# Kernel optimization log

Hardware: AMD Instinct MI355X
Metric: run time of the kernel (lower is better)

Reference implementation:

```python
import jax, jax.numpy as jnp
import numpy as np

# Dimensions (AlphaFold-scale IPA / GeometricFrameAttention)
B, N = 1, 768
C_S, C_Z, C_H, H, PQ, PV = 384, 128, 16, 12, 4, 8
INF = 1e9
EPS = 1e-8
SOFTPLUS_INV_1 = 0.541324854612918  # gfa_point_weights_init_


def quat_to_rot(q):
    """Unit-normalize quaternions [..., 4] -> rotation matrices [..., 3, 3]."""
    q = q / jnp.linalg.norm(q, axis=-1, keepdims=True)
    w, x, y, z = q[..., 0], q[..., 1], q[..., 2], q[..., 3]
    R = jnp.stack([
        1 - 2 * (y * y + z * z), 2 * (x * y - w * z), 2 * (x * z + w * y),
        2 * (x * y + w * z), 1 - 2 * (x * x + z * z), 2 * (y * z - w * x),
        2 * (x * z - w * y), 2 * (y * z + w * x), 1 - 2 * (x * x + y * y),
    ], axis=-1)
    return R.reshape(q.shape[:-1] + (3, 3))


def setup_inputs() -> dict:
    key = jax.random.key(0)
    ks = jax.random.split(key, 12)

    def lin(k, out_d, in_d):
        return jax.random.normal(k, (out_d, in_d), jnp.float32) * (1.0 / np.sqrt(in_d))

    out_in = H * C_H + H * PV * 4 + H * C_Z  # o + o_pt(x,y,z) + o_pt_norm + o_pair
    inp = {
        "s": jax.random.normal(ks[0], (B, N, C_S), jnp.float32),
        "z": jax.random.normal(ks[1], (B, N, N, C_Z), jnp.float32),
        "rot": quat_to_rot(jax.random.normal(ks[2], (B, N, 4), jnp.float32)),
        "trans": jax.random.normal(ks[3], (B, N, 3), jnp.float32),
        "mask": jnp.ones((B, N), jnp.float32),
        "Wq": lin(ks[4], H * C_H, C_S),
        "bq": jnp.zeros((H * C_H,), jnp.float32),
        "Wkv": lin(ks[5], H * 2 * C_H, C_S),
        "bkv": jnp.zeros((H * 2 * C_H,), jnp.float32),
        "Wqp": lin(ks[6], H * PQ * 3, C_S),
        "bqp": jnp.zeros((H * PQ * 3,), jnp.float32),
        "Wkvp": lin(ks[7], H * (PQ + PV) * 3, C_S),
        "bkvp": jnp.zeros((H * (PQ + PV) * 3,), jnp.float32),
        "Wb": lin(ks[8], H, C_Z),
        "bb": jnp.zeros((H,), jnp.float32),
        "head_w": jnp.full((H,), SOFTPLUS_INV_1, jnp.float32),
        "Wout": lin(ks[9], C_S, out_in),
        "bout": jnp.zeros((C_S,), jnp.float32),
    }
    return inp


def _forward(s, z, rot, trans, mask, Wq, bq, Wkv, bkv, Wqp, bqp, Wkvp, bkvp,
             Wb, bb, head_w, Wout, bout):
    Bn, Nn, _ = s.shape
    # scalar q/k/v
    q = (s @ Wq.T + bq).reshape(Bn, Nn, H, C_H)
    kv = (s @ Wkv.T + bkv).reshape(Bn, Nn, H, 2 * C_H)
    k, v = kv[..., :C_H], kv[..., C_H:]
    # point q/k/v: local frame -> global frame (x_glob = R x_loc + t)
    q_pts = (s @ Wqp.T + bqp).reshape(Bn, Nn, H * PQ, 3)
    q_pts = (jnp.einsum('bnxy,bnpy->bnpx', rot, q_pts) + trans[:, :, None]).reshape(Bn, Nn, H, PQ, 3)
    kv_pts = (s @ Wkvp.T + bkvp).reshape(Bn, Nn, H * (PQ + PV), 3)
    kv_pts = (jnp.einsum('bnxy,bnpy->bnpx', rot, kv_pts) + trans[:, :, None]).reshape(Bn, Nn, H, PQ + PV, 3)
    k_pts, v_pts = kv_pts[..., :PQ, :], kv_pts[..., PQ:, :]
    # pair bias [B,N,N,H] -> [B,H,N,N]
    bias = z @ Wb.T + bb
    a = jnp.einsum('bihc,bjhc->bhij', q, k) * np.float32(np.sqrt(1.0 / (3 * C_H)))
    a = a + np.float32(np.sqrt(1.0 / 3.0)) * jnp.transpose(bias, (0, 3, 1, 2))
    # point distance term: sum_p |q_p - k_p|^2 = |q|^2 + |k|^2 - 2 q.k (no [B,N,N,H,P,3] tensor)
    q2 = jnp.sum(q_pts ** 2, axis=(-1, -2))  # [B,N,H]
    k2 = jnp.sum(k_pts ** 2, axis=(-1, -2))
    qk = jnp.einsum('bihpc,bjhpc->bhij', q_pts, k_pts)
    d2 = q2.transpose(0, 2, 1)[..., :, None] + k2.transpose(0, 2, 1)[..., None, :] - 2.0 * qk
    hw = jax.nn.softplus(head_w) * np.float32(np.sqrt(2.0 / (27.0 * PQ)))  # sqrt(1/(3*(PQ*9/2)))
    a = a - 0.5 * hw[None, :, None, None] * d2
    # mask bias
    sq_mask = mask[..., :, None] * mask[..., None, :]
    a = a + (INF * (sq_mask - 1.0))[:, None]
    a = jax.nn.softmax(a, axis=-1)  # [B,H,N,N]
    # outputs
    o = jnp.einsum('bhij,bjhc->bihc', a, v).reshape(Bn, Nn, H * C_H)
    o_pt = jnp.einsum('bhij,bjhpc->bihpc', a, v_pts)  # global frame
    o_pt = jnp.einsum('bnyx,bnhpy->bnhpx', rot, o_pt - trans[:, :, None, None])  # back to local
    o_pt_norm = jnp.sqrt(jnp.sum(o_pt ** 2, axis=-1) + EPS).reshape(Bn, Nn, H * PV)
    o_pt_flat = jnp.moveaxis(o_pt, -1, -3).reshape(Bn, Nn, 3 * H * PV)  # coord-major like unbind+cat
    o_pair = jnp.einsum('bhij,bijc->bihc', a, z).reshape(Bn, Nn, H * C_Z)
    cat = jnp.concatenate([o, o_pt_flat, o_pt_norm, o_pair], axis=-1)
    return cat @ Wout.T + bout


def reference(s, z, rot, trans, mask, Wq, bq, Wkv, bkv, Wqp, bqp, Wkvp, bkvp,
              Wb, bb, head_w, Wout, bout):
    return _forward(s, z, rot, trans, mask, Wq, bq, Wkv, bkv, Wqp, bqp,
                    Wkvp, bkvp, Wb, bb, head_w, Wout, bout)
```

## Files before the change

### kernel.cpp

```cpp
#include <hip/hip_runtime.h>
#include <math.h>

#define NN 768
#define CS 384
#define CZ 128
#define CH 16
#define HH 12
#define PQ 4
#define PV 8
#define OUTIN 2112

#define SC_QK 0.14433756729740643f
#define SC_B  0.57735026918962576f
#define SC_HW 0.13608276348795434f

__global__ __launch_bounds__(256) void kproj(
    const float* __restrict__ s,
    const float* __restrict__ Wq,  const float* __restrict__ bq,
    const float* __restrict__ Wkv, const float* __restrict__ bkv,
    const float* __restrict__ Wqp, const float* __restrict__ bqp,
    const float* __restrict__ Wkvp,const float* __restrict__ bkvp,
    float* __restrict__ q, float* __restrict__ kT, float* __restrict__ vallT,
    float* __restrict__ qpr, float* __restrict__ kvpr)
{
    __shared__ float s_lds[8*384];
    int n0 = blockIdx.x * 8;
    int t = threadIdx.x;
    for (int idx = t; idx < 8*384; idx += 256)
        s_lds[idx] = s[(n0 + idx/384)*384 + (idx%384)];
    __syncthreads();

    int o = blockIdx.y * 128 + (t & 127);
    int ng = t >> 7;
    const float* wrow; float bias;
    if (o < 192)      { wrow = Wq   + o*384;       bias = bq[o]; }
    else if (o < 576) { wrow = Wkv  + (o-192)*384; bias = bkv[o-192]; }
    else if (o < 720) { wrow = Wqp  + (o-576)*384; bias = bqp[o-576]; }
    else              { wrow = Wkvp + (o-720)*384; bias = bkvp[o-720]; }

    float acc[4] = {bias, bias, bias, bias};
    const float4* wr4 = reinterpret_cast<const float4*>(wrow);
    for (int c4 = 0; c4 < 96; ++c4) {
        float4 w = wr4[c4];
        #pragma unroll
        for (int nn = 0; nn < 4; ++nn) {
            const float* sr = &s_lds[(ng*4+nn)*384 + c4*4];
            acc[nn] = fmaf(w.x, sr[0], acc[nn]);
            acc[nn] = fmaf(w.y, sr[1], acc[nn]);
            acc[nn] = fmaf(w.z, sr[2], acc[nn]);
            acc[nn] = fmaf(w.w, sr[3], acc[nn]);
        }
    }
    #pragma unroll
    for (int nn = 0; nn < 4; ++nn) {
        int n = n0 + ng*4 + nn;
        float v = acc[nn];
        if (o < 192)      q[n*192 + o] = v;
        else if (o < 576) {
            int oo = o - 192, h = oo >> 5, cc = oo & 31;
            if (cc < 16) kT[(h*NN + n)*16 + cc] = v;
            else         vallT[(size_t)(h*40 + (cc-16))*NN + n] = v;
        }
        else if (o < 720) qpr[n*144 + (o-576)] = v;
        else              kvpr[n*432 + (o-720)] = v;
    }
}

__global__ __launch_bounds__(192) void krot(
    const float* __restrict__ rot, const float* __restrict__ trans,
    const float* __restrict__ qpr, const float* __restrict__ kvpr,
    float* __restrict__ qp, float* __restrict__ kpT, float* __restrict__ vallT)
{
    int n = blockIdx.x;
    __shared__ float R[9], T[3];
    int t = threadIdx.x;
    if (t < 9) R[t] = rot[n*9 + t];
    if (t < 3) T[t] = trans[n*3 + t];
    __syncthreads();

    const float* src = (t < 48) ? (qpr + n*144 + t*3) : (kvpr + n*432 + (t-48)*3);
    float x = src[0], y = src[1], z = src[2];
    float wx = R[0]*x + R[1]*y + R[2]*z + T[0];
    float wy = R[3]*x + R[4]*y + R[5]*z + T[1];
    float wz = R[6]*x + R[7]*y + R[8]*z + T[2];
    if (t < 48) {
        float* d = qp + n*144 + t*3;
        d[0]=wx; d[1]=wy; d[2]=wz;
    } else {
        int pi = t - 48, h = pi/12, pp = pi%12;
        if (pp < 4) {
            float* d = kpT + (h*NN+n)*12 + pp*3;
            d[0]=wx; d[1]=wy; d[2]=wz;
        } else {
            int ch = h*40 + 16 + (pp-4)*3;
            vallT[(size_t)(ch+0)*NN + n] = wx;
            vallT[(size_t)(ch+1)*NN + n] = wy;
            vallT[(size_t)(ch+2)*NN + n] = wz;
        }
    }
}

__global__ __launch_bounds__(256) void kqk(
    const float* __restrict__ kT, const float* __restrict__ kpT,
    const float* __restrict__ q, const float* __restrict__ qp,
    const float* __restrict__ mask, const float* __restrict__ head_w,
    const float* __restrict__ bb, float* __restrict__ lqd)
{
    const int h = blockIdx.z;
    const int j0 = blockIdx.x * 128;
    const int i0 = blockIdx.y * 32;
    __shared__ float kt_l[16][132], kp_l[12][132];
    __shared__ float q_l[32][16], qp_l[32][12];
    __shared__ float mi_l[32], mj_l[128];
    const int t = threadIdx.x;
    for (int idx = t; idx < 2048; idx += 256) {
        int j = idx >> 4, c = idx & 15;
        kt_l[c][j] = kT[(size_t)(h*NN + j0 + j)*16 + c];
    }
    for (int idx = t; idx < 1536; idx += 256) {
        int j = idx / 12, e = idx - j*12;
        kp_l[e][j] = kpT[(size_t)(h*NN + j0 + j)*12 + e];
    }
    for (int idx = t; idx < 512; idx += 256) {
        int ii = idx >> 4, c = idx & 15;
        q_l[ii][c] = q[(i0+ii)*192 + h*16 + c];
    }
    for (int idx = t; idx < 384; idx += 256) {
        int ii = idx / 12, e = idx - ii*12;
        qp_l[ii][e] = qp[(i0+ii)*144 + h*12 + e];
    }
    if (t < 32)  mi_l[t] = mask[i0 + t];
    if (t < 128) mj_l[t] = mask[j0 + t];
    const float hwh = log1pf(expf(head_w[h])) * SC_HW;
    const float bbh = bb[h];
    __syncthreads();

    const int jl = t & 127, ig = t >> 7;
    const float mj = mj_l[jl];
    #pragma unroll 4
    for (int ii = 0; ii < 16; ++ii) {
        const int il = ig*16 + ii;
        float qk = 0.f;
        #pragma unroll
        for (int c = 0; c < 16; ++c) qk = fmaf(kt_l[c][jl], q_l[il][c], qk);
        float d2 = 0.f;
        #pragma unroll
        for (int e = 0; e < 12; ++e) { float d = qp_l[il][e] - kp_l[e][jl]; d2 = fmaf(d, d, d2); }
        float mt = 1e9f * (mi_l[il]*mj - 1.0f);
        float lg = fmaf(qk, SC_QK, fmaf(-0.5f*hwh, d2, bbh)) + mt;
        lqd[((size_t)h*NN + i0 + il)*NN + j0 + jl] = lg;
    }
}

__global__ __launch_bounds__(256, 4) void kbias(
    const float* __restrict__ z, const float* __restrict__ Wb,
    const float* __restrict__ lqd, float* __restrict__ g_out,
    float* __restrict__ mrow)
{
    __shared__ float4 zt4[64][32];

    const int i = blockIdx.x, t = threadIdx.x;
    const int w = t >> 6, l = t & 63, h0 = w*3;
    const int h0u = __builtin_amdgcn_readfirstlane(h0);
    const float4* __restrict__ wbh = (const float4*)(Wb + h0u*CZ);

    const float4* __restrict__ zg = (const float4*)(z + (size_t)i*NN*CZ);
    float4 stg[8];
    #pragma unroll
    for (int k = 0; k < 8; ++k) stg[k] = zg[k*256 + t];
    #pragma unroll
    for (int k = 0; k < 8; ++k) {
        int slot = k*256 + t, j = slot >> 5, c4 = slot & 31;
        zt4[j][c4 ^ (j & 7)] = stg[k];
    }

    float m0 = -1e30f, m1 = -1e30f, m2 = -1e30f;
    const int swl = l & 7;

    for (int tile = 0; tile < 12; ++tile) {
        __syncthreads();
        if (tile + 1 < 12) {
            #pragma unroll
            for (int k = 0; k < 8; ++k) stg[k] = zg[(tile+1)*2048 + k*256 + t];
        }
        const int j = tile*64 + l;
        float lq0 = lqd[((size_t)(h0+0)*NN + i)*NN + j];
        float lq1 = lqd[((size_t)(h0+1)*NN + i)*NN + j];
        float lq2 = lqd[((size_t)(h0+2)*NN + i)*NN + j];
        float b0 = 0.f, b1 = 0.f, b2 = 0.f;
        #pragma unroll
        for (int c4 = 0; c4 < 32; ++c4) {
            float4 zv = zt4[l][c4 ^ swl];
            float4 w0 = wbh[c4];
            float4 w1 = wbh[32 + c4];
            float4 w2 = wbh[64 + c4];
            b0 = fmaf(zv.x,w0.x,b0); b0 = fmaf(zv.y,w0.y,b0); b0 = fmaf(zv.z,w0.z,b0); b0 = fmaf(zv.w,w0.w,b0);
            b1 = fmaf(zv.x,w1.x,b1); b1 = fmaf(zv.y,w1.y,b1); b1 = fmaf(zv.z,w1.z,b1); b1 = fmaf(zv.w,w1.w,b1);
            b2 = fmaf(zv.x,w2.x,b2); b2 = fmaf(zv.y,w2.y,b2); b2 = fmaf(zv.z,w2.z,b2); b2 = fmaf(zv.w,w2.w,b2);
        }
        float g0 = fmaf(b0, SC_B, lq0);
        float g1 = fmaf(b1, SC_B, lq1);
        float g2 = fmaf(b2, SC_B, lq2);
        g_out[((size_t)(h0+0)*NN + i)*NN + j] = g0;
        g_out[((size_t)(h0+1)*NN + i)*NN + j] = g1;
        g_out[((size_t)(h0+2)*NN + i)*NN + j] = g2;
        m0 = fmaxf(m0, g0); m1 = fmaxf(m1, g1); m2 = fmaxf(m2, g2);
        __syncthreads();
        if (tile + 1 < 12) {
            #pragma unroll
            for (int k = 0; k < 8; ++k) {
                int slot = k*256 + t, jj = slot >> 5, c4 = slot & 31;
                zt4[jj][c4 ^ (jj & 7)] = stg[k];
            }
        }
    }

    #pragma unroll
    for (int off = 32; off >= 1; off >>= 1) {
        m0 = fmaxf(m0, __shfl_xor(m0, off, 64));
        m1 = fmaxf(m1, __shfl_xor(m1, off, 64));
        m2 = fmaxf(m2, __shfl_xor(m2, off, 64));
    }
    if (l == 0) {
        mrow[(h0+0)*NN + i] = m0;
        mrow[(h0+1)*NN + i] = m1;
        mrow[(h0+2)*NN + i] = m2;
    }
}

__global__ __launch_bounds__(256, 4) void kfin(
    const float* __restrict__ z, const float* __restrict__ vallT,
    const float* __restrict__ g, const float* __restrict__ mrow,
    const float* __restrict__ rot, const float* __restrict__ trans,
    float* __restrict__ cat)
{
    __shared__ float an_l[12][776];
    __shared__ float sred[12][4];
    __shared__ float sinv[12];
    __shared__ float optl[12][24];
    __shared__ float R[9], T[3];
    const int i = blockIdx.x, t = threadIdx.x, w = t >> 6, l = t & 63;
    if (t < 9) R[t] = rot[i*9 + t];
    if (t < 3) T[t] = trans[i*3 + t];

    float ps[12];
    #pragma unroll
    for (int h = 0; h < 12; ++h) ps[h] = 0.f;
    #pragma unroll
    for (int h = 0; h < 12; ++h) {
        const float mh = mrow[h*NN + i];
        const float* gr = g + ((size_t)h*NN + i)*NN;
        #pragma unroll
        for (int k = 0; k < 3; ++k) {
            int j = k*256 + t;
            float p = __expf(gr[j] - mh);
            an_l[h][j] = p;
            ps[h] += p;
        }
    }
    #pragma unroll
    for (int h = 0; h < 12; ++h) {
        float s = ps[h];
        #pragma unroll
        for (int off = 32; off >= 1; off >>= 1) s += __shfl_xor(s, off, 64);
        if (l == 0) sred[h][w] = s;
    }
    __syncthreads();
    if (t < 12) sinv[t] = 1.0f / (sred[t][0] + sred[t][1] + sred[t][2] + sred[t][3]);
    __syncthreads();

    {
        const int h0 = w*3, jo = l >> 5, c4 = l & 31;
        const float4* __restrict__ zr = (const float4*)(z + (size_t)i*NN*CZ);
        float a0x=0,a0y=0,a0z=0,a0w=0, a1x=0,a1y=0,a1z=0,a1w=0, a2x=0,a2y=0,a2z=0,a2w=0;
        #pragma unroll 4
        for (int jb = 0; jb < 384; ++jb) {
            const int j = jb*2 + jo;
            float4 zv = zr[(size_t)j*32 + c4];
            float p0 = an_l[h0+0][j], p1 = an_l[h0+1][j], p2 = an_l[h0+2][j];
            a0x = fmaf(p0, zv.x, a0x); a0y = fmaf(p0, zv.y, a0y);
            a0z = fmaf(p0, zv.z, a0z); a0w = fmaf(p0, zv.w, a0w);
            a1x = fmaf(p1, zv.x, a1x); a1y = fmaf(p1, zv.y, a1y);
            a1z = fmaf(p1, zv.z, a1z); a1w = fmaf(p1, zv.w, a1w);
            a2x = fmaf(p2, zv.x, a2x); a2y = fmaf(p2, zv.y, a2y);
            a2z = fmaf(p2, zv.z, a2z); a2w = fmaf(p2, zv.w, a2w);
        }
        a0x += __shfl_xor(a0x, 32, 64); a0y += __shfl_xor(a0y, 32, 64);
        a0z += __shfl_xor(a0z, 32, 64); a0w += __shfl_xor(a0w, 32, 64);
        a1x += __shfl_xor(a1x, 32, 64); a1y += __shfl_xor(a1y, 32, 64);
        a1z += __shfl_xor(a1z, 32, 64); a1w += __shfl_xor(a1w, 32, 64);
        a2x += __shfl_xor(a2x, 32, 64); a2y += __shfl_xor(a2y, 32, 64);
        a2z += __shfl_xor(a2z, 32, 64); a2w += __shfl_xor(a2w, 32, 64);
        if (jo == 0) {
            float* crow = cat + (size_t)i*OUTIN + 576;
            float i0v = sinv[h0+0], i1v = sinv[h0+1], i2v = sinv[h0+2];
            float4 o0; o0.x = a0x*i0v; o0.y = a0y*i0v; o0.z = a0z*i0v; o0.w = a0w*i0v;
            float4 o1; o1.x = a1x*i1v; o1.y = a1y*i1v; o1.z = a1z*i1v; o1.w = a1w*i1v;
            float4 o2; o2.x = a2x*i2v; o2.y = a2y*i2v; o2.z = a2z*i2v; o2.w = a2w*i2v;
            *(float4*)(crow + (h0+0)*128 + c4*4) = o0;
            *(float4*)(crow + (h0+1)*128 + c4*4) = o1;
            *(float4*)(crow + (h0+2)*128 + c4*4) = o2;
        }
    }

    float* crow = cat + (size_t)i*OUTIN;
    for (int cc = 0; cc < 120; ++cc) {
        const int ch = w*120 + cc;
        const int h = ch / 40, e = ch % 40;
        const float2* __restrict__ vr = (const float2*)(vallT + (size_t)ch*NN);
        const float2* __restrict__ pr = (const float2*)(&an_l[h][0]);
        float ax = 0.f, ay = 0.f;
        #pragma unroll
        for (int jc = 0; jc < 6; ++jc) {
            float2 v = vr[jc*64 + l];
            float2 p = pr[jc*64 + l];
            ax = fmaf(p.x, v.x, ax);
            ay = fmaf(p.y, v.y, ay);
        }
        float sv = ax + ay;
        #pragma unroll
        for (int off = 32; off >= 1; off >>= 1) sv += __shfl_xor(sv, off, 64);
        if (l == 0) {
            float val = sv * sinv[h];
            if (e < 16) crow[h*16 + e] = val;
            else        optl[h][e-16] = val;
        }
    }
    __syncthreads();
    if (t < 96) {
        int h = t >> 3, p = t & 7;
        float wx = optl[h][p*3+0] - T[0];
        float wy = optl[h][p*3+1] - T[1];
        float wz = optl[h][p*3+2] - T[2];
        crow[192 + 0*96 + h*8 + p] = R[0]*wx + R[3]*wy + R[6]*wz;
        crow[192 + 1*96 + h*8 + p] = R[1]*wx + R[4]*wy + R[7]*wz;
        crow[192 + 2*96 + h*8 + p] = R[2]*wx + R[5]*wy + R[8]*wz;
        crow[480 + h*8 + p] = sqrtf(fmaf(wx,wx,fmaf(wy,wy,wz*wz)) + 1e-8f);
    }
}

__global__ __launch_bounds__(256) void koutp(
    const float* __restrict__ cat, const float* __restrict__ Wout,
    float* __restrict__ ptmp)
{
    __shared__ float ct[32][36];
    __shared__ float wt[64][36];
    const int n0 = blockIdx.x * 32, o0 = blockIdx.y * 64;
    const int k0 = blockIdx.z * 352;
    const int t = threadIdx.x;
    const int tn = (t >> 4) * 2;
    const int to = t & 15;

    float a00=0,a01=0,a02=0,a03=0, a10=0,a11=0,a12=0,a13=0;

    for (int c = 0; c < 11; ++c) {
        __syncthreads();
        #pragma unroll
        for (int u = 0; u < 4; ++u) {
            int idx = u*256 + t, r = idx >> 5, cc = idx & 31;
            ct[r][cc] = cat[(size_t)(n0 + r)*OUTIN + k0 + c*32 + cc];
        }
        #pragma unroll
        for (int u = 0; u < 8; ++u) {
            int idx = u*256 + t, r = idx >> 5, cc = idx & 31;
            wt[r][cc] = Wout[(size_t)(o0 + r)*OUTIN + k0 + c*32 + cc];
        }
        __syncthreads();
        #pragma unroll
        for (int kk = 0; kk < 32; kk += 4) {
            float4 c0 = *(const float4*)&ct[tn][kk];
            float4 c1 = *(const float4*)&ct[tn+1][kk];
            float4 w0 = *(const float4*)&wt[to][kk];
            float4 w1 = *(const float4*)&wt[to+16][kk];
            float4 w2 = *(const float4*)&wt[to+32][kk];
            float4 w3 = *(const float4*)&wt[to+48][kk];
            a00 = fmaf(c0.x,w0.x,a00); a00 = fmaf(c0.y,w0.y,a00); a00 = fmaf(c0.z,w0.z,a00); a00 = fmaf(c0.w,w0.w,a00);
            a01 = fmaf(c0.x,w1.x,a01); a01 = fmaf(c0.y,w1.y,a01); a01 = fmaf(c0.z,w1.z,a01); a01 = fmaf(c0.w,w1.w,a01);
            a02 = fmaf(c0.x,w2.x,a02); a02 = fmaf(c0.y,w2.y,a02); a02 = fmaf(c0.z,w2.z,a02); a02 = fmaf(c0.w,w2.w,a02);
            a03 = fmaf(c0.x,w3.x,a03); a03 = fmaf(c0.y,w3.y,a03); a03 = fmaf(c0.z,w3.z,a03); a03 = fmaf(c0.w,w3.w,a03);
            a10 = fmaf(c1.x,w0.x,a10); a10 = fmaf(c1.y,w0.y,a10); a10 = fmaf(c1.z,w0.z,a10); a10 = fmaf(c1.w,w0.w,a10);
            a11 = fmaf(c1.x,w1.x,a11); a11 = fmaf(c1.y,w1.y,a11); a11 = fmaf(c1.z,w1.z,a11); a11 = fmaf(c1.w,w1.w,a11);
            a12 = fmaf(c1.x,w2.x,a12); a12 = fmaf(c1.y,w2.y,a12); a12 = fmaf(c1.z,w2.z,a12); a12 = fmaf(c1.w,w2.w,a12);
            a13 = fmaf(c1.x,w3.x,a13); a13 = fmaf(c1.y,w3.y,a13); a13 = fmaf(c1.z,w3.z,a13); a13 = fmaf(c1.w,w3.w,a13);
        }
    }
    float* pb = ptmp + (size_t)blockIdx.z * (NN*384);
    pb[(size_t)(n0+tn+0)*384 + o0+to+ 0] = a00;
    pb[(size_t)(n0+tn+0)*384 + o0+to+16] = a01;
    pb[(size_t)(n0+tn+0)*384 + o0+to+32] = a02;
    pb[(size_t)(n0+tn+0)*384 + o0+to+48] = a03;
    pb[(size_t)(n0+tn+1)*384 + o0+to+ 0] = a10;
    pb[(size_t)(n0+tn+1)*384 + o0+to+16] = a11;
    pb[(size_t)(n0+tn+1)*384 + o0+to+32] = a12;
    pb[(size_t)(n0+tn+1)*384 + o0+to+48] = a13;
}

__global__ __launch_bounds__(256) void kred(
    const float* __restrict__ ptmp, const float* __restrict__ bout,
    float* __restrict__ out)
{
    int idx = blockIdx.x * 256 + threadIdx.x;
    int o = idx % 384;
    float v = bout[o];
    #pragma unroll
    for (int s = 0; s < 6; ++s) v += ptmp[(size_t)s*(NN*384) + idx];
    out[idx] = v;
}

extern "C" void kernel_launch(void* const* d_in, const int* in_sizes, int n_in,
                              void* d_out, int out_size, void* d_ws, size_t ws_size,
                              hipStream_t stream) {
    const float* s      = (const float*)d_in[0];
    const float* z      = (const float*)d_in[1];
    const float* rot    = (const float*)d_in[2];
    const float* trans  = (const float*)d_in[3];
    const float* mask   = (const float*)d_in[4];
    const float* Wq     = (const float*)d_in[5];
    const float* bq     = (const float*)d_in[6];
    const float* Wkv    = (const float*)d_in[7];
    const float* bkv    = (const float*)d_in[8];
    const float* Wqp    = (const float*)d_in[9];
    const float* bqp    = (const float*)d_in[10];
    const float* Wkvp   = (const float*)d_in[11];
    const float* bkvp   = (const float*)d_in[12];
    const float* Wb     = (const float*)d_in[13];
    const float* bb     = (const float*)d_in[14];
    const float* head_w = (const float*)d_in[15];
    const float* Wout   = (const float*)d_in[16];
    const float* bout   = (const float*)d_in[17];
    float* out = (float*)d_out;
    float* ws  = (float*)d_ws;

    float* q     = ws;
    float* kT    = ws + 147456;
    float* kpT   = ws + 294912;
    float* vallT = ws + 405504;
    float* qp    = ws + 774144;
    float* qpr   = ws + 884736;
    float* kvpr  = ws + 995328;
    float* mrow  = ws + 1327104;
    float* cat   = ws + 1336320;
    float* lqd   = ws + 2958336;
    float* gbuf  = ws + 10036224;
    float* ptmp  = ws + 17114112;

    kproj<<<dim3(96, 9), 256, 0, stream>>>(s, Wq, bq, Wkv, bkv, Wqp, bqp, Wkvp, bkvp,
                                           q, kT, vallT, qpr, kvpr);
    krot<<<dim3(768), 192, 0, stream>>>(rot, trans, qpr, kvpr, qp, kpT, vallT);
    kqk<<<dim3(6, 24, 12), 256, 0, stream>>>(kT, kpT, q, qp, mask, head_w, bb, lqd);
    kbias<<<dim3(768), 256, 0, stream>>>(z, Wb, lqd, gbuf, mrow);
    kfin<<<dim3(768), 256, 0, stream>>>(z, vallT, gbuf, mrow, rot, trans, cat);
    koutp<<<dim3(24, 6, 6), 256, 0, stream>>>(cat, Wout, ptmp);
    kred<<<dim3(1152), 256, 0, stream>>>(ptmp, bout, out);
}
```

Before: 436.4 us.

## Store logits head-innermost and restructure bias and softmax kernels around it

Logits and the biased scores are now stored as [i][j][h] instead of [h][i][j]. The qk kernel loops over all 12 heads inside one block. The bias kernel uses 16-lane groups per key, each reducing the full 128-channel z row against all heads held in registers via shuffles, with no LDS staging. The final kernel reads all 12 heads per key with float4 loads and processes four keys per iteration in the pair-aggregation loop, which cuts LDS loads. The intent is fewer passes and better vectorisation over the large z and score tensors. The cost is many cross-lane shuffles, heavy register use and only one active lane per group for the score stores.

Result: slower. 588.8 us (+34.9%).

```diff
diff --git a/kernel.cpp b/kernel.cpp
--- a/kernel.cpp
+++ b/kernel.cpp
@@ -106,49 +106,49 @@
     const float* __restrict__ mask, const float* __restrict__ head_w,
     const float* __restrict__ bb, float* __restrict__ lqd)
 {
-    const int h = blockIdx.z;
-    const int j0 = blockIdx.x * 128;
+    const int j0 = blockIdx.x * 64;
     const int i0 = blockIdx.y * 32;
-    __shared__ float kt_l[16][132], kp_l[12][132];
-    __shared__ float q_l[32][16], qp_l[32][12];
-    __shared__ float mi_l[32], mj_l[128];
+    __shared__ float ktl[64][17], kpl[64][13];
+    __shared__ float ql[32][17],  qpl[32][13];
+    __shared__ float mi_l[32], mj_l[64];
     const int t = threadIdx.x;
-    for (int idx = t; idx < 2048; idx += 256) {
-        int j = idx >> 4, c = idx & 15;
-        kt_l[c][j] = kT[(size_t)(h*NN + j0 + j)*16 + c];
-    }
-    for (int idx = t; idx < 1536; idx += 256) {
-        int j = idx / 12, e = idx - j*12;
-        kp_l[e][j] = kpT[(size_t)(h*NN + j0 + j)*12 + e];
-    }
-    for (int idx = t; idx < 512; idx += 256) {
-        int ii = idx >> 4, c = idx & 15;
-        q_l[ii][c] = q[(i0+ii)*192 + h*16 + c];
-    }
-    for (int idx = t; idx < 384; idx += 256) {
-        int ii = idx / 12, e = idx - ii*12;
-        qp_l[ii][e] = qp[(i0+ii)*144 + h*12 + e];
-    }
-    if (t < 32)  mi_l[t] = mask[i0 + t];
-    if (t < 128) mj_l[t] = mask[j0 + t];
-    const float hwh = log1pf(expf(head_w[h])) * SC_HW;
-    const float bbh = bb[h];
-    __syncthreads();
-
-    const int jl = t & 127, ig = t >> 7;
-    const float mj = mj_l[jl];
-    #pragma unroll 4
-    for (int ii = 0; ii < 16; ++ii) {
-        const int il = ig*16 + ii;
-        float qk = 0.f;
-        #pragma unroll
-        for (int c = 0; c < 16; ++c) qk = fmaf(kt_l[c][jl], q_l[il][c], qk);
-        float d2 = 0.f;
-        #pragma unroll
-        for (int e = 0; e < 12; ++e) { float d = qp_l[il][e] - kp_l[e][jl]; d2 = fmaf(d, d, d2); }
-        float mt = 1e9f * (mi_l[il]*mj - 1.0f);
-        float lg = fmaf(qk, SC_QK, fmaf(-0.5f*hwh, d2, bbh)) + mt;
-        lqd[((size_t)h*NN + i0 + il)*NN + j0 + jl] = lg;
+    if (t < 32) mi_l[t] = mask[i0 + t];
+    if (t < 64) mj_l[t] = mask[j0 + t];
+
+    const int jl = t & 63, wv = t >> 6;
+
+    for (int h = 0; h < 12; ++h) {
+        __syncthreads();
+        for (int idx = t; idx < 1024; idx += 256)
+            ktl[idx >> 4][idx & 15] = kT[(size_t)(h*NN + j0 + (idx >> 4))*16 + (idx & 15)];
+        for (int idx = t; idx < 768; idx += 256) {
+            int r = idx / 12, e = idx - r*12;
+            kpl[r][e] = kpT[(size_t)(h*NN + j0 + r)*12 + e];
+        }
+        for (int idx = t; idx < 512; idx += 256)
+            ql[idx >> 4][idx & 15] = q[(i0 + (idx >> 4))*192 + h*16 + (idx & 15)];
+        for (int idx = t; idx < 384; idx += 256) {
+            int r = idx / 12, e = idx - r*12;
+            qpl[r][e] = qp[(i0 + r)*144 + h*12 + e];
+        }
+        __syncthreads();
+
+        const float hwh = log1pf(expf(head_w[h])) * SC_HW;
+        const float bbh = bb[h] * SC_B;
+        const float mj = mj_l[jl];
+        #pragma unroll
+        for (int k = 0; k < 8; ++k) {
+            const int il = wv*8 + k;
+            float qk = 0.f;
+            #pragma unroll
+            for (int c = 0; c < 16; ++c) qk = fmaf(ktl[jl][c], ql[il][c], qk);
+            float d2 = 0.f;
+            #pragma unroll
+            for (int e = 0; e < 12; ++e) { float d = qpl[il][e] - kpl[jl][e]; d2 = fmaf(d, d, d2); }
+            float mt = 1e9f * (mi_l[il]*mj - 1.0f);
+            float lg = fmaf(qk, SC_QK, fmaf(-0.5f*hwh, d2, bbh)) + mt;
+            lqd[((size_t)(i0+il)*NN + j0 + jl)*12 + h] = lg;
+        }
     }
 }
 
@@ -157,74 +157,88 @@
     const float* __restrict__ lqd, float* __restrict__ g_out,
     float* __restrict__ mrow)
 {
-    __shared__ float4 zt4[64][32];
-
+    __shared__ float mxl[16][12];
     const int i = blockIdx.x, t = threadIdx.x;
-    const int w = t >> 6, l = t & 63, h0 = w*3;
-    const int h0u = __builtin_amdgcn_readfirstlane(h0);
-    const float4* __restrict__ wbh = (const float4*)(Wb + h0u*CZ);
-
-    const float4* __restrict__ zg = (const float4*)(z + (size_t)i*NN*CZ);
-    float4 stg[8];
+    const int w = t >> 6, l = t & 63;
+    const int grp = l >> 4, cl = l & 15;
+
+    float4 wva[12], wvb[12];
     #pragma unroll
-    for (int k = 0; k < 8; ++k) stg[k] = zg[k*256 + t];
+    for (int h = 0; h < 12; ++h) {
+        const float4* wp = (const float4*)(Wb + h*CZ + cl*8);
+        wva[h] = wp[0];
+        wvb[h] = wp[1];
+    }
+
+    float mx[12];
     #pragma unroll
-    for (int k = 0; k < 8; ++k) {
-        int slot = k*256 + t, j = slot >> 5, c4 = slot & 31;
-        zt4[j][c4 ^ (j & 7)] = stg[k];
-    }
-
-    float m0 = -1e30f, m1 = -1e30f, m2 = -1e30f;
-    const int swl = l & 7;
-
-    for (int tile = 0; tile < 12; ++tile) {
-        __syncthreads();
-        if (tile + 1 < 12) {
-            #pragma unroll
-            for (int k = 0; k < 8; ++k) stg[k] = zg[(tile+1)*2048 + k*256 + t];
-        }
-        const int j = tile*64 + l;
-        float lq0 = lqd[((size_t)(h0+0)*NN + i)*NN + j];
-        float lq1 = lqd[((size_t)(h0+1)*NN + i)*NN + j];
-        float lq2 = lqd[((size_t)(h0+2)*NN + i)*NN + j];
-        float b0 = 0.f, b1 = 0.f, b2 = 0.f;
-        #pragma unroll
-        for (int c4 = 0; c4 < 32; ++c4) {
-            float4 zv = zt4[l][c4 ^ swl];
-            float4 w0 = wbh[c4];
-            float4 w1 = wbh[32 + c4];
-            float4 w2 = wbh[64 + c4];
-            b0 = fmaf(zv.x,w0.x,b0); b0 = fmaf(zv.y,w0.y,b0); b0 = fmaf(zv.z,w0.z,b0); b0 = fmaf(zv.w,w0.w,b0);
-            b1 = fmaf(zv.x,w1.x,b1); b1 = fmaf(zv.y,w1.y,b1); b1 = fmaf(zv.z,w1.z,b1); b1 = fmaf(zv.w,w1.w,b1);
-            b2 = fmaf(zv.x,w2.x,b2); b2 = fmaf(zv.y,w2.y,b2); b2 = fmaf(zv.z,w2.z,b2); b2 = fmaf(zv.w,w2.w,b2);
-        }
-        float g0 = fmaf(b0, SC_B, lq0);
-        float g1 = fmaf(b1, SC_B, lq1);
-        float g2 = fmaf(b2, SC_B, lq2);
-        g_out[((size_t)(h0+0)*NN + i)*NN + j] = g0;
-        g_out[((size_t)(h0+1)*NN + i)*NN + j] = g1;
-        g_out[((size_t)(h0+2)*NN + i)*NN + j] = g2;
-        m0 = fmaxf(m0, g0); m1 = fmaxf(m1, g1); m2 = fmaxf(m2, g2);
-        __syncthreads();
-        if (tile + 1 < 12) {
-            #pragma unroll
-            for (int k = 0; k < 8; ++k) {
-                int slot = k*256 + t, jj = slot >> 5, c4 = slot & 31;
-                zt4[jj][c4 ^ (jj & 7)] = stg[k];
-            }
-        }
-    }
-
-    #pragma unroll
-    for (int off = 32; off >= 1; off >>= 1) {
-        m0 = fmaxf(m0, __shfl_xor(m0, off, 64));
-        m1 = fmaxf(m1, __shfl_xor(m1, off, 64));
-        m2 = fmaxf(m2, __shfl_xor(m2, off, 64));
-    }
-    if (l == 0) {
-        mrow[(h0+0)*NN + i] = m0;
-        mrow[(h0+1)*NN + i] = m1;
-        mrow[(h0+2)*NN + i] = m2;
+    for (int h = 0; h < 12; ++h) mx[h] = -1e30f;
+
+    for (int it = 0; it < 48; ++it) {
+        const int j = it*16 + w*4 + grp;
+        const float4* zr4 = (const float4*)(z + ((size_t)i*NN + j)*CZ) + cl*2;
+        float4 za = zr4[0], zb = zr4[1];
+
+        float b[12];
+        #pragma unroll
+        for (int h = 0; h < 12; ++h) {
+            float acc;
+            acc = za.x*wva[h].x;
+            acc = fmaf(za.y, wva[h].y, acc);
+            acc = fmaf(za.z, wva[h].z, acc);
+            acc = fmaf(za.w, wva[h].w, acc);
+            acc = fmaf(zb.x, wvb[h].x, acc);
+            acc = fmaf(zb.y, wvb[h].y, acc);
+            acc = fmaf(zb.z, wvb[h].z, acc);
+            acc = fmaf(zb.w, wvb[h].w, acc);
+            b[h] = acc;
+        }
+        #pragma unroll
+        for (int h = 0; h < 12; ++h) {
+            b[h] += __shfl_xor(b[h], 1, 16);
+            b[h] += __shfl_xor(b[h], 2, 16);
+            b[h] += __shfl_xor(b[h], 4, 16);
+            b[h] += __shfl_xor(b[h], 8, 16);
+        }
+        if (cl == 0) {
+            const float4* lq4 = (const float4*)(lqd + ((size_t)i*NN + j)*12);
+            float4 qa = lq4[0], qb = lq4[1], qc = lq4[2];
+            float g0  = fmaf(b[0],  SC_B, qa.x);
+            float g1  = fmaf(b[1],  SC_B, qa.y);
+            float g2  = fmaf(b[2],  SC_B, qa.z);
+            float g3  = fmaf(b[3],  SC_B, qa.w);
+            float g4  = fmaf(b[4],  SC_B, qb.x);
+            float g5  = fmaf(b[5],  SC_B, qb.y);
+            float g6  = fmaf(b[6],  SC_B, qb.z);
+            float g7  = fmaf(b[7],  SC_B, qb.w);
+            float g8  = fmaf(b[8],  SC_B, qc.x);
+            float g9  = fmaf(b[9],  SC_B, qc.y);
+            float g10 = fmaf(b[10], SC_B, qc.z);
+            float g11 = fmaf(b[11], SC_B, qc.w);
+            float4* go = (float4*)(g_out + ((size_t)i*NN + j)*12);
+            float4 oa; oa.x = g0; oa.y = g1; oa.z = g2;  oa.w = g3;
+            float4 ob; ob.x = g4; ob.y = g5; ob.z = g6;  ob.w = g7;
+            float4 oc; oc.x = g8; oc.y = g9; oc.z = g10; oc.w = g11;
+            go[0] = oa; go[1] = ob; go[2] = oc;
+            mx[0] = fmaxf(mx[0], g0);  mx[1] = fmaxf(mx[1], g1);
+            mx[2] = fmaxf(mx[2], g2);  mx[3] = fmaxf(mx[3], g3);
+            mx[4] = fmaxf(mx[4], g4);  mx[5] = fmaxf(mx[5], g5);
+            mx[6] = fmaxf(mx[6], g6);  mx[7] = fmaxf(mx[7], g7);
+            mx[8] = fmaxf(mx[8], g8);  mx[9] = fmaxf(mx[9], g9);
+            mx[10] = fmaxf(mx[10], g10); mx[11] = fmaxf(mx[11], g11);
+        }
+    }
+
+    if (cl == 0) {
+        #pragma unroll
+        for (int h = 0; h < 12; ++h) mxl[w*4 + grp][h] = mx[h];
+    }
+    __syncthreads();
+    if (t < 12) {
+        float m = mxl[0][t];
+        #pragma unroll
+        for (int r = 1; r < 16; ++r) m = fmaxf(m, mxl[r][t]);
+        mrow[t*NN + i] = m;
     }
 }
 
@@ -237,33 +251,50 @@
     __shared__ float an_l[12][776];
     __shared__ float sred[12][4];
     __shared__ float sinv[12];
+    __shared__ float m_lds[12];
     __shared__ float optl[12][24];
     __shared__ float R[9], T[3];
     const int i = blockIdx.x, t = threadIdx.x, w = t >> 6, l = t & 63;
     if (t < 9) R[t] = rot[i*9 + t];
     if (t < 3) T[t] = trans[i*3 + t];
-
-    float ps[12];
+    if (t >= 16 && t < 28) m_lds[t-16] = mrow[(t-16)*NN + i];
+    __syncthreads();
+
+    float m0 = m_lds[0], m1 = m_lds[1], m2 = m_lds[2],  m3 = m_lds[3];
+    float m4 = m_lds[4], m5 = m_lds[5], m6 = m_lds[6],  m7 = m_lds[7];
+    float m8 = m_lds[8], m9 = m_lds[9], m10 = m_lds[10], m11 = m_lds[11];
+
+    float4 psA = {0,0,0,0}, psB = {0,0,0,0}, psC = {0,0,0,0};
+    const float4* gr4 = (const float4*)(g + (size_t)i*NN*12);
     #pragma unroll
-    for (int h = 0; h < 12; ++h) ps[h] = 0.f;
-    #pragma unroll
-    for (int h = 0; h < 12; ++h) {
-        const float mh = mrow[h*NN + i];
-        const float* gr = g + ((size_t)h*NN + i)*NN;
-        #pragma unroll
-        for (int k = 0; k < 3; ++k) {
-            int j = k*256 + t;
-            float p = __expf(gr[j] - mh);
-            an_l[h][j] = p;
-            ps[h] += p;
-        }
-    }
-    #pragma unroll
-    for (int h = 0; h < 12; ++h) {
-        float s = ps[h];
-        #pragma unroll
-        for (int off = 32; off >= 1; off >>= 1) s += __shfl_xor(s, off, 64);
-        if (l == 0) sred[h][w] = s;
+    for (int jj = 0; jj < 3; ++jj) {
+        const int j = jj*256 + t;
+        float4 ga = gr4[j*3 + 0];
+        float4 gb = gr4[j*3 + 1];
+        float4 gc = gr4[j*3 + 2];
+        float p0  = __expf(ga.x - m0),  p1  = __expf(ga.y - m1);
+        float p2  = __expf(ga.z - m2),  p3  = __expf(ga.w - m3);
+        float p4  = __expf(gb.x - m4),  p5  = __expf(gb.y - m5);
+        float p6  = __expf(gb.z - m6),  p7  = __expf(gb.w - m7);
+        float p8  = __expf(gc.x - m8),  p9  = __expf(gc.y - m9);
+        float p10 = __expf(gc.z - m10), p11 = __expf(gc.w - m11);
+        an_l[0][j] = p0;  an_l[1][j] = p1;  an_l[2][j] = p2;  an_l[3][j] = p3;
+        an_l[4][j] = p4;  an_l[5][j] = p5;  an_l[6][j] = p6;  an_l[7][j] = p7;
+        an_l[8][j] = p8;  an_l[9][j] = p9;  an_l[10][j] = p10; an_l[11][j] = p11;
+        psA.x += p0;  psA.y += p1;  psA.z += p2;  psA.w += p3;
+        psB.x += p4;  psB.y += p5;  psB.z += p6;  psB.w += p7;
+        psC.x += p8;  psC.y += p9;  psC.z += p10; psC.w += p11;
+    }
+    {
+        float sums[12] = {psA.x, psA.y, psA.z, psA.w, psB.x, psB.y, psB.z, psB.w,
+                          psC.x, psC.y, psC.z, psC.w};
+        #pragma unroll
+        for (int h = 0; h < 12; ++h) {
+            float s = sums[h];
+            #pragma unroll
+            for (int off = 32; off >= 1; off >>= 1) s += __shfl_xor(s, off, 64);
+            if (l == 0) sred[h][w] = s;
+        }
     }
     __syncthreads();
     if (t < 12) sinv[t] = 1.0f / (sred[t][0] + sred[t][1] + sred[t][2] + sred[t][3]);
@@ -271,32 +302,56 @@
 
     {
         const int h0 = w*3, jo = l >> 5, c4 = l & 31;
-        const float4* __restrict__ zr = (const float4*)(z + (size_t)i*NN*CZ);
-        float a0x=0,a0y=0,a0z=0,a0w=0, a1x=0,a1y=0,a1z=0,a1w=0, a2x=0,a2y=0,a2z=0,a2w=0;
-        #pragma unroll 4
-        for (int jb = 0; jb < 384; ++jb) {
-            const int j = jb*2 + jo;
-            float4 zv = zr[(size_t)j*32 + c4];
-            float p0 = an_l[h0+0][j], p1 = an_l[h0+1][j], p2 = an_l[h0+2][j];
-            a0x = fmaf(p0, zv.x, a0x); a0y = fmaf(p0, zv.y, a0y);
-            a0z = fmaf(p0, zv.z, a0z); a0w = fmaf(p0, zv.w, a0w);
-            a1x = fmaf(p1, zv.x, a1x); a1y = fmaf(p1, zv.y, a1y);
-            a1z = fmaf(p1, zv.z, a1z); a1w = fmaf(p1, zv.w, a1w);
-            a2x = fmaf(p2, zv.x, a2x); a2y = fmaf(p2, zv.y, a2y);
-            a2z = fmaf(p2, zv.z, a2z); a2w = fmaf(p2, zv.w, a2w);
-        }
-        a0x += __shfl_xor(a0x, 32, 64); a0y += __shfl_xor(a0y, 32, 64);
-        a0z += __shfl_xor(a0z, 32, 64); a0w += __shfl_xor(a0w, 32, 64);
-        a1x += __shfl_xor(a1x, 32, 64); a1y += __shfl_xor(a1y, 32, 64);
-        a1z += __shfl_xor(a1z, 32, 64); a1w += __shfl_xor(a1w, 32, 64);
-        a2x += __shfl_xor(a2x, 32, 64); a2y += __shfl_xor(a2y, 32, 64);
-        a2z += __shfl_xor(a2z, 32, 64); a2w += __shfl_xor(a2w, 32, 64);
+        const float4* __restrict__ zr = (const float4*)(z + (size_t)i*NN*CZ) + c4;
+        float4 a0 = {0,0,0,0}, a1 = {0,0,0,0}, a2 = {0,0,0,0};
+        for (int jb = 0; jb < 96; ++jb) {
+            const int j0 = jb*8 + jo*4;
+            float4 z0 = zr[(size_t)(j0+0)*32];
+            float4 z1 = zr[(size_t)(j0+1)*32];
+            float4 z2 = zr[(size_t)(j0+2)*32];
+            float4 z3 = zr[(size_t)(j0+3)*32];
+            float4 pA = *(const float4*)&an_l[h0+0][j0];
+            float4 pB = *(const float4*)&an_l[h0+1][j0];
+            float4 pC = *(const float4*)&an_l[h0+2][j0];
+            a0.x = fmaf(pA.x, z0.x, a0.x); a0.y = fmaf(pA.x, z0.y, a0.y);
+            a0.z = fmaf(pA.x, z0.z, a0.z); a0.w = fmaf(pA.x, z0.w, a0.w);
+            a0.x = fmaf(pA.y, z1.x, a0.x); a0.y = fmaf(pA.y, z1.y, a0.y);
+            a0.z = fmaf(pA.y, z1.z, a0.z); a0.w = fmaf(pA.y, z1.w, a0.w);
+            a0.x = fmaf(pA.z, z2.x, a0.x); a0.y = fmaf(pA.z, z2.y, a0.y);
+            a0.z = fmaf(pA.z, z2.z, a0.z); a0.w = fmaf(pA.z, z2.w, a0.w);
+            a0.x = fmaf(pA.w, z3.x, a0.x); a0.y = fmaf(pA.w, z3.y, a0.y);
+            a0.z = fmaf(pA.w, z3.z, a0.z); a0.w = fmaf(pA.w, z3.w, a0.w);
+
+            a1.x = fmaf(pB.x, z0.x, a1.x); a1.y = fmaf(pB.x, z0.y, a1.y);
+            a1.z = fmaf(pB.x, z0.z, a1.z); a1.w = fmaf(pB.x, z0.w, a1.w);
+            a1.x = fmaf(pB.y, z1.x, a1.x); a1.y = fmaf(pB.y, z1.y, a1.y);
+            a1.z = fmaf(pB.y, z1.z, a1.z); a1.w = fmaf(pB.y, z1.w, a1.w);
+            a1.x = fmaf(pB.z, z2.x, a1.x); a1.y = fmaf(pB.z, z2.y, a1.y);
+            a1.z = fmaf(pB.z, z2.z, a1.z); a1.w = fmaf(pB.z, z2.w, a1.w);
+            a1.x = fmaf(pB.w, z3.x, a1.x); a1.y = fmaf(pB.w, z3.y, a1.y);
+            a1.z = fmaf(pB.w, z3.z, a1.z); a1.w = fmaf(pB.w, z3.w, a1.w);
+
+            a2.x = fmaf(pC.x, z0.x, a2.x); a2.y = fmaf(pC.x, z0.y, a2.y);
+            a2.z = fmaf(pC.x, z0.z, a2.z); a2.w = fmaf(pC.x, z0.w, a2.w);
+            a2.x = fmaf(pC.y, z1.x, a2.x); a2.y = fmaf(pC.y, z1.y, a2.y);
+            a2.z = fmaf(pC.y, z1.z, a2.z); a2.w = fmaf(pC.y, z1.w, a2.w);
+            a2.x = fmaf(pC.z, z2.x, a2.x); a2.y = fmaf(pC.z, z2.y, a2.y);
+            a2.z = fmaf(pC.z, z2.z, a2.z); a2.w = fmaf(pC.z, z2.w, a2.w);
+            a2.x = fmaf(pC.w, z3.x, a2.x); a2.y = fmaf(pC.w, z3.y, a2.y);
+            a2.z = fmaf(pC.w, z3.z, a2.z); a2.w = fmaf(pC.w, z3.w, a2.w);
+        }
+        a0.x += __shfl_xor(a0.x, 32, 64); a0.y += __shfl_xor(a0.y, 32, 64);
+        a0.z += __shfl_xor(a0.z, 32, 64); a0.w += __shfl_xor(a0.w, 32, 64);
+        a1.x += __shfl_xor(a1.x, 32, 64); a1.y += __shfl_xor(a1.y, 32, 64);
+        a1.z += __shfl_xor(a1.z, 32, 64); a1.w += __shfl_xor(a1.w, 32, 64);
+        a2.x += __shfl_xor(a2.x, 32, 64); a2.y += __shfl_xor(a2.y, 32, 64);
+        a2.z += __shfl_xor(a2.z, 32, 64); a2.w += __shfl_xor(a2.w, 32, 64);
         if (jo == 0) {
             float* crow = cat + (size_t)i*OUTIN + 576;
             float i0v = sinv[h0+0], i1v = sinv[h0+1], i2v = sinv[h0+2];
-            float4 o0; o0.x = a0x*i0v; o0.y = a0y*i0v; o0.z = a0z*i0v; o0.w = a0w*i0v;
-            float4 o1; o1.x = a1x*i1v; o1.y = a1y*i1v; o1.z = a1z*i1v; o1.w = a1w*i1v;
-            float4 o2; o2.x = a2x*i2v; o2.y = a2y*i2v; o2.z = a2z*i2v; o2.w = a2w*i2v;
+            float4 o0; o0.x = a0.x*i0v; o0.y = a0.y*i0v; o0.z = a0.z*i0v; o0.w = a0.w*i0v;
+            float4 o1; o1.x = a1.x*i1v; o1.y = a1.y*i1v; o1.z = a1.z*i1v; o1.w = a1.w*i1v;
+            float4 o2; o2.x = a2.x*i2v; o2.y = a2.y*i2v; o2.z = a2.z*i2v; o2.w = a2.w*i2v;
             *(float4*)(crow + (h0+0)*128 + c4*4) = o0;
             *(float4*)(crow + (h0+1)*128 + c4*4) = o1;
             *(float4*)(crow + (h0+2)*128 + c4*4) = o2;
@@ -447,7 +502,7 @@
     kproj<<<dim3(96, 9), 256, 0, stream>>>(s, Wq, bq, Wkv, bkv, Wqp, bqp, Wkvp, bkvp,
                                            q, kT, vallT, qpr, kvpr);
     krot<<<dim3(768), 192, 0, stream>>>(rot, trans, qpr, kvpr, qp, kpT, vallT);
-    kqk<<<dim3(6, 24, 12), 256, 0, stream>>>(kT, kpT, q, qp, mask, head_w, bb, lqd);
+    kqk<<<dim3(12, 24), 256, 0, stream>>>(kT, kpT, q, qp, mask, head_w, bb, lqd);
     kbias<<<dim3(768), 256, 0, stream>>>(z, Wb, lqd, gbuf, mrow);
     kfin<<<dim3(768), 256, 0, stream>>>(z, vallT, gbuf, mrow, rot, trans, cat);
     koutp<<<dim3(24, 6, 6), 256, 0, stream>>>(cat, Wout, ptmp);
```
